# Kernel tuning notes

Measured on AMD Instinct MI355X. Metric: run time of the kernel, lower is better.

The kernel has to match this reference:

```python
import jax, jax.numpy as jnp
import numpy as np

N, F, U, H = 4096, 512, 64, 8
EDGE_PROB = 0.01
NEG_MASK = -10e9  # matches keras-gat masking constant
LRELU_SLOPE = 0.2


def setup_inputs() -> dict:
    key = jax.random.key(0)
    kX, kA, kI, kW, kS, kN, kB = jax.random.split(key, 7)
    X = jax.random.normal(kX, (1, N, F), dtype=jnp.float32)
    # sparse binary adjacency with self loops (layer expects preprocessed self-loops)
    A = (jax.random.uniform(kA, (N, N)) < EDGE_PROB).astype(jnp.float32)
    A = jnp.maximum(A, jnp.eye(N, dtype=jnp.float32))
    out_indices = jax.random.randint(kI, (1, 128), 0, N).astype(jnp.int64)
    scale_w = 1.0 / np.sqrt(F)
    scale_a = 1.0 / np.sqrt(U)
    W = jax.random.normal(kW, (H, F, U), dtype=jnp.float32) * scale_w
    a_self = jax.random.normal(kS, (H, U), dtype=jnp.float32) * scale_a
    a_neigh = jax.random.normal(kN, (H, U), dtype=jnp.float32) * scale_a
    bias = jax.random.normal(kB, (H, U), dtype=jnp.float32) * 0.1
    return {"X": X, "out_indices": out_indices, "A": A, "W": W,
            "a_self": a_self, "a_neigh": a_neigh, "bias": bias}


def reference(X, out_indices, A, W, a_self, a_neigh, bias):
    x = X[0]  # [N, F] (batch dim of 1)
    # per-head linear transform: [H, N, U]
    h = jnp.einsum('nf,hfu->hnu', x, W)
    # additive attention logits: f_self[i] + f_neigh[j]
    f_self = jnp.einsum('hnu,hu->hn', h, a_self)    # [H, N]
    f_neigh = jnp.einsum('hnu,hu->hn', h, a_neigh)  # [H, N]
    scores = f_self[:, :, None] + f_neigh[:, None, :]  # [H, N, N]
    scores = jax.nn.leaky_relu(scores, negative_slope=LRELU_SLOPE)
    # mask non-edges (standard, non-saliency path): dense += -10e9 * (1 - A)
    scores = scores + NEG_MASK * (1.0 - A)[None, :, :]
    attn = jax.nn.softmax(scores, axis=-1)  # [H, N, N]
    # weighted aggregation + bias
    out = jnp.einsum('hnm,hmu->hnu', attn, h) + bias[:, None, :]  # [H, N, U]
    # concat heads: [N, H*U], then activation (relu)
    out = jnp.transpose(out, (1, 0, 2)).reshape(N, H * U)
    out = jax.nn.relu(out)
    return out[None, :, :]  # [1, N, H*U]; final_layer=False -> all nodes
```

## Files before the change

### kernel.cpp

```cpp
#include <hip/hip_runtime.h>
#include <hip/hip_bf16.h>

#define N_NODES 4096
#define F_DIM   512
#define U_DIM   64
#define H_HEADS 8
#define C_DIM   512
#define LRELU_S 0.2f
#define MAXE    128
#define GEMM_BLOCKS 512

typedef __attribute__((ext_vector_type(8))) short bf16x8;
typedef __attribute__((ext_vector_type(4))) float f32x4;

__device__ inline unsigned short f2bf(float f) {
  union { float f; unsigned u; } v; v.f = f;
  unsigned r = v.u + 0x7FFFu + ((v.u >> 16) & 1u);
  return (unsigned short)(r >> 16);
}
__device__ inline float bf2f(unsigned short b) {
  union { unsigned u; float f; } v; v.u = ((unsigned)b) << 16;
  return v.f;
}

__global__ __launch_bounds__(256) void front_kernel(
    const float* __restrict__ X, const float* __restrict__ W,
    const float* __restrict__ A, const float* __restrict__ a_self,
    const float* __restrict__ a_neigh, unsigned short* __restrict__ hb,
    float* __restrict__ fsT, float* __restrict__ fnT, int* __restrict__ deg,
    unsigned short* __restrict__ nbr) {
  __shared__ unsigned short As[64][72];
  __shared__ unsigned short Bs[64][72];
  __shared__ int wsum[4];

  const int t    = threadIdx.x;
  const int lane = t & 63;
  const int w    = t >> 6;

  if ((int)blockIdx.x < GEMM_BLOCKS) {
    const int mblk = blockIdx.x & 63;
    const int head = blockIdx.x >> 6;
    const int m0   = mblk * 64;
    const float* Wh = W + (size_t)head * F_DIM * U_DIM;

    const int wr = w >> 1, wc = w & 1;
    const int arow = t >> 2;
    const int akc  = (t & 3) * 16;
    const int bu   = t & 63;
    const int bjc  = (t >> 6) * 16;

    f32x4 acc[2][2] = {};

    for (int k0 = 0; k0 < F_DIM; k0 += 64) {
      {
        const float* src = X + (size_t)(m0 + arow) * F_DIM + k0 + akc;
        float4 f0 = ((const float4*)src)[0];
        float4 f1 = ((const float4*)src)[1];
        float4 f2 = ((const float4*)src)[2];
        float4 f3 = ((const float4*)src)[3];
        bf16x8 u0 = {(short)f2bf(f0.x), (short)f2bf(f0.y), (short)f2bf(f0.z),
                     (short)f2bf(f0.w), (short)f2bf(f1.x), (short)f2bf(f1.y),
                     (short)f2bf(f1.z), (short)f2bf(f1.w)};
        bf16x8 u1 = {(short)f2bf(f2.x), (short)f2bf(f2.y), (short)f2bf(f2.z),
                     (short)f2bf(f2.w), (short)f2bf(f3.x), (short)f2bf(f3.y),
                     (short)f2bf(f3.z), (short)f2bf(f3.w)};
        *(bf16x8*)&As[arow][akc]     = u0;
        *(bf16x8*)&As[arow][akc + 8] = u1;
      }
      {
        float bv[16];
#pragma unroll
        for (int j = 0; j < 16; ++j)
          bv[j] = Wh[(size_t)(k0 + bjc + j) * U_DIM + bu];
        bf16x8 w0 = {(short)f2bf(bv[0]), (short)f2bf(bv[1]), (short)f2bf(bv[2]),
                     (short)f2bf(bv[3]), (short)f2bf(bv[4]), (short)f2bf(bv[5]),
                     (short)f2bf(bv[6]), (short)f2bf(bv[7])};
        bf16x8 w1 = {(short)f2bf(bv[8]),  (short)f2bf(bv[9]),
                     (short)f2bf(bv[10]), (short)f2bf(bv[11]),
                     (short)f2bf(bv[12]), (short)f2bf(bv[13]),
                     (short)f2bf(bv[14]), (short)f2bf(bv[15])};
        *(bf16x8*)&Bs[bu][bjc]     = w0;
        *(bf16x8*)&Bs[bu][bjc + 8] = w1;
      }
      __syncthreads();

      const int r  = lane & 15;
      const int ko = (lane >> 4) * 8;
#pragma unroll
      for (int kk = 0; kk < 2; ++kk) {
        bf16x8 af0 = *(const bf16x8*)&As[wr * 32 + r][kk * 32 + ko];
        bf16x8 af1 = *(const bf16x8*)&As[wr * 32 + 16 + r][kk * 32 + ko];
        bf16x8 bf0 = *(const bf16x8*)&Bs[wc * 32 + r][kk * 32 + ko];
        bf16x8 bf1 = *(const bf16x8*)&Bs[wc * 32 + 16 + r][kk * 32 + ko];
        acc[0][0] = __builtin_amdgcn_mfma_f32_16x16x32_bf16(af0, bf0, acc[0][0], 0, 0, 0);
        acc[0][1] = __builtin_amdgcn_mfma_f32_16x16x32_bf16(af0, bf1, acc[0][1], 0, 0, 0);
        acc[1][0] = __builtin_amdgcn_mfma_f32_16x16x32_bf16(af1, bf0, acc[1][0], 0, 0, 0);
        acc[1][1] = __builtin_amdgcn_mfma_f32_16x16x32_bf16(af1, bf1, acc[1][1], 0, 0, 0);
      }
      __syncthreads();
    }

#pragma unroll
    for (int mi = 0; mi < 2; ++mi) {
#pragma unroll
      for (int ni = 0; ni < 2; ++ni) {
        const int rb = wr * 32 + mi * 16 + (lane >> 4) * 4;
        const int cl = wc * 32 + ni * 16 + (lane & 15);
#pragma unroll
        for (int reg = 0; reg < 4; ++reg) {
          unsigned short hv = f2bf(acc[mi][ni][reg]);
          hb[(size_t)(m0 + rb + reg) * C_DIM + head * U_DIM + cl] = hv;
          As[rb + reg][cl] = hv;
        }
      }
    }
    __syncthreads();
    if (t < 128) {
      const int r = t & 63;
      const float* avec = (t >= 64) ? a_neigh + head * U_DIM
                                    : a_self + head * U_DIM;
      float s = 0.f;
#pragma unroll
      for (int u = 0; u < 64; ++u) s += bf2f(As[r][u]) * avec[u];
      float* dst = (t >= 64) ? fnT : fsT;
      dst[(size_t)(m0 + r) * H_HEADS + head] = s;
    }
  } else {
    const int i = (int)blockIdx.x - GEMM_BLOCKS;
    const float* Aq = A + (size_t)i * N_NODES + w * 1024;
    float4 v0 = *(const float4*)(Aq +   0 + 4 * lane);
    float4 v1 = *(const float4*)(Aq + 256 + 4 * lane);
    float4 v2 = *(const float4*)(Aq + 512 + 4 * lane);
    float4 v3 = *(const float4*)(Aq + 768 + 4 * lane);

    unsigned long long mk[16];
    mk[ 0] = __ballot(v0.x != 0.f); mk[ 1] = __ballot(v0.y != 0.f);
    mk[ 2] = __ballot(v0.z != 0.f); mk[ 3] = __ballot(v0.w != 0.f);
    mk[ 4] = __ballot(v1.x != 0.f); mk[ 5] = __ballot(v1.y != 0.f);
    mk[ 6] = __ballot(v1.z != 0.f); mk[ 7] = __ballot(v1.w != 0.f);
    mk[ 8] = __ballot(v2.x != 0.f); mk[ 9] = __ballot(v2.y != 0.f);
    mk[10] = __ballot(v2.z != 0.f); mk[11] = __ballot(v2.w != 0.f);
    mk[12] = __ballot(v3.x != 0.f); mk[13] = __ballot(v3.y != 0.f);
    mk[14] = __ballot(v3.z != 0.f); mk[15] = __ballot(v3.w != 0.f);

    int cnt = 0;
#pragma unroll
    for (int q = 0; q < 16; ++q) cnt += __popcll(mk[q]);
    if (lane == 0) wsum[w] = cnt;
    __syncthreads();

    int base = 0;
#pragma unroll
    for (int k = 0; k < 4; ++k)
      if (k < w) base += wsum[k];
    const int total = wsum[0] + wsum[1] + wsum[2] + wsum[3];

    const unsigned long long lt  = (lane == 63) ? 0x7FFFFFFFFFFFFFFFULL
                                                : ((1ULL << lane) - 1ULL);
    const unsigned long long bit = 1ULL << lane;
    unsigned short* nrow = nbr + (size_t)i * MAXE;
#pragma unroll
    for (int q = 0; q < 16; ++q) {
      if (mk[q] & bit) {
        const int pos = base + (int)__popcll(mk[q] & lt);
        if (pos < MAXE)
          nrow[pos] =
              (unsigned short)(w * 1024 + (q >> 2) * 256 + 4 * lane + (q & 3));
      }
      base += (int)__popcll(mk[q]);
    }
    if (t == 0) deg[i] = (total > MAXE) ? MAXE : total;
  }
}

__global__ __launch_bounds__(256) void attn_kernel(
    const unsigned short* __restrict__ hb, const float* __restrict__ fsT,
    const float* __restrict__ fnT, const float* __restrict__ bias,
    const int* __restrict__ deg, const unsigned short* __restrict__ nbr,
    float* __restrict__ out) {
  __shared__ int   eidx[4][MAXE];
  __shared__ float p[4][MAXE][9];

  const int t    = threadIdx.x;
  const int lane = t & 63;
  const int w    = t >> 6;
  const int i    = blockIdx.x * 4 + w;
  const int E    = deg[i];

  float fsv[8];
  {
    float4 a = *(const float4*)(fsT + (size_t)i * H_HEADS);
    float4 b = *(const float4*)(fsT + (size_t)i * H_HEADS + 4);
    fsv[0]=a.x; fsv[1]=a.y; fsv[2]=a.z; fsv[3]=a.w;
    fsv[4]=b.x; fsv[5]=b.y; fsv[6]=b.z; fsv[7]=b.w;
  }

  float pmax[8];
#pragma unroll
  for (int h = 0; h < 8; ++h) pmax[h] = -1e30f;
  for (int e = lane; e < E; e += 64) {
    const int j = (int)nbr[(size_t)i * MAXE + e];
    eidx[w][e] = j;
    float4 a = *(const float4*)(fnT + (size_t)j * H_HEADS);
    float4 b = *(const float4*)(fnT + (size_t)j * H_HEADS + 4);
    float fnv[8] = {a.x, a.y, a.z, a.w, b.x, b.y, b.z, b.w};
#pragma unroll
    for (int h = 0; h < 8; ++h) {
      float sc = fsv[h] + fnv[h];
      sc = (sc > 0.f) ? sc : LRELU_S * sc;
      p[w][e][h] = sc;
      pmax[h] = fmaxf(pmax[h], sc);
    }
  }
#pragma unroll
  for (int h = 0; h < 8; ++h)
#pragma unroll
    for (int off = 32; off > 0; off >>= 1)
      pmax[h] = fmaxf(pmax[h], __shfl_xor(pmax[h], off));

  float psum[8] = {};
  for (int e = lane; e < E; e += 64) {
#pragma unroll
    for (int h = 0; h < 8; ++h) {
      float ex = __expf(p[w][e][h] - pmax[h]);
      p[w][e][h] = ex;
      psum[h] += ex;
    }
  }
#pragma unroll
  for (int h = 0; h < 8; ++h)
#pragma unroll
    for (int off = 32; off > 0; off >>= 1) psum[h] += __shfl_xor(psum[h], off);

  __syncthreads();

  const int cbase = 8 * lane;
  const int hl = lane >> 3;
  float acc[8] = {};
  for (int e = 0; e < E; ++e) {
    const int j = eidx[w][e];
    uint4 v = *(const uint4*)(hb + (size_t)j * C_DIM + cbase);
    const float pe = p[w][e][hl];
    acc[0] += pe * bf2f((unsigned short)(v.x & 0xFFFFu));
    acc[1] += pe * bf2f((unsigned short)(v.x >> 16));
    acc[2] += pe * bf2f((unsigned short)(v.y & 0xFFFFu));
    acc[3] += pe * bf2f((unsigned short)(v.y >> 16));
    acc[4] += pe * bf2f((unsigned short)(v.z & 0xFFFFu));
    acc[5] += pe * bf2f((unsigned short)(v.z >> 16));
    acc[6] += pe * bf2f((unsigned short)(v.w & 0xFFFFu));
    acc[7] += pe * bf2f((unsigned short)(v.w >> 16));
  }
  float sum = psum[0];
#pragma unroll
  for (int h = 1; h < 8; ++h)
    if (hl == h) sum = psum[h];
  const float inv = 1.0f / sum;

  float4 b0 = *(const float4*)(bias + cbase);
  float4 b1 = *(const float4*)(bias + cbase + 4);
  float4 o0, o1;
  o0.x = fmaxf(acc[0] * inv + b0.x, 0.f);
  o0.y = fmaxf(acc[1] * inv + b0.y, 0.f);
  o0.z = fmaxf(acc[2] * inv + b0.z, 0.f);
  o0.w = fmaxf(acc[3] * inv + b0.w, 0.f);
  o1.x = fmaxf(acc[4] * inv + b1.x, 0.f);
  o1.y = fmaxf(acc[5] * inv + b1.y, 0.f);
  o1.z = fmaxf(acc[6] * inv + b1.z, 0.f);
  o1.w = fmaxf(acc[7] * inv + b1.w, 0.f);
  *(float4*)(out + (size_t)i * C_DIM + cbase)     = o0;
  *(float4*)(out + (size_t)i * C_DIM + cbase + 4) = o1;
}

extern "C" void kernel_launch(void* const* d_in, const int* in_sizes, int n_in,
                              void* d_out, int out_size, void* d_ws,
                              size_t ws_size, hipStream_t stream) {
  const float* X       = (const float*)d_in[0];
  const float* A       = (const float*)d_in[2];
  const float* W       = (const float*)d_in[3];
  const float* a_self  = (const float*)d_in[4];
  const float* a_neigh = (const float*)d_in[5];
  const float* bias    = (const float*)d_in[6];
  float* out = (float*)d_out;

  unsigned short* hb = (unsigned short*)d_ws;
  float* fsT = (float*)(hb + (size_t)N_NODES * C_DIM);
  float* fnT = fsT + (size_t)H_HEADS * N_NODES;
  int* deg   = (int*)(fnT + (size_t)H_HEADS * N_NODES);
  unsigned short* nbr = (unsigned short*)(deg + N_NODES);

  front_kernel<<<GEMM_BLOCKS + N_NODES, 256, 0, stream>>>(
      X, W, A, a_self, a_neigh, hb, fsT, fnT, deg, nbr);

  attn_kernel<<<N_NODES / 4, 256, 0, stream>>>(hb, fsT, fnT, bias, deg, nbr,
                                               out);
}
```

Measured before the change: 41.54 us.

## Split each attention node across two wavefronts, each handling four heads

The attention kernel now assigns two wavefronts per destination node instead of one. Each wavefront computes softmax for four of the eight heads and aggregates half of the output columns with 4-wide bf16 loads. This doubles the grid size and halves per-thread serial work, which should expose more memory-level parallelism for the gather. In exchange it adds a block-level sync for neighbor index staging and duplicates some index and score work across the two wavefronts.

Result: slower. 42.99 us (+3.5%).

```diff
diff --git a/kernel.cpp b/kernel.cpp
--- a/kernel.cpp
+++ b/kernel.cpp
@@ -178,97 +178,87 @@
     const float* __restrict__ fnT, const float* __restrict__ bias,
     const int* __restrict__ deg, const unsigned short* __restrict__ nbr,
     float* __restrict__ out) {
-  __shared__ int   eidx[4][MAXE];
-  __shared__ float p[4][MAXE][9];
+  __shared__ int   eidx[2][MAXE];
+  __shared__ float p[2][MAXE][9];
 
   const int t    = threadIdx.x;
   const int lane = t & 63;
   const int w    = t >> 6;
-  const int i    = blockIdx.x * 4 + w;
+  const int nd   = w >> 1;
+  const int wn   = w & 1;
+  const int i    = blockIdx.x * 2 + nd;
   const int E    = deg[i];
 
-  float fsv[8];
   {
-    float4 a = *(const float4*)(fsT + (size_t)i * H_HEADS);
-    float4 b = *(const float4*)(fsT + (size_t)i * H_HEADS + 4);
-    fsv[0]=a.x; fsv[1]=a.y; fsv[2]=a.z; fsv[3]=a.w;
-    fsv[4]=b.x; fsv[5]=b.y; fsv[6]=b.z; fsv[7]=b.w;
-  }
-
-  float pmax[8];
-#pragma unroll
-  for (int h = 0; h < 8; ++h) pmax[h] = -1e30f;
+    const int e = wn * 64 + lane;
+    if (e < E) eidx[nd][e] = (int)nbr[(size_t)i * MAXE + e];
+  }
+  __syncthreads();
+
+  float4 fsq = *(const float4*)(fsT + (size_t)i * H_HEADS + wn * 4);
+  const float fsv[4] = {fsq.x, fsq.y, fsq.z, fsq.w};
+
+  float pmax[4] = {-1e30f, -1e30f, -1e30f, -1e30f};
   for (int e = lane; e < E; e += 64) {
-    const int j = (int)nbr[(size_t)i * MAXE + e];
-    eidx[w][e] = j;
-    float4 a = *(const float4*)(fnT + (size_t)j * H_HEADS);
-    float4 b = *(const float4*)(fnT + (size_t)j * H_HEADS + 4);
-    float fnv[8] = {a.x, a.y, a.z, a.w, b.x, b.y, b.z, b.w};
-#pragma unroll
-    for (int h = 0; h < 8; ++h) {
+    const int j = eidx[nd][e];
+    float4 a = *(const float4*)(fnT + (size_t)j * H_HEADS + wn * 4);
+    float fnv[4] = {a.x, a.y, a.z, a.w};
+#pragma unroll
+    for (int h = 0; h < 4; ++h) {
       float sc = fsv[h] + fnv[h];
       sc = (sc > 0.f) ? sc : LRELU_S * sc;
-      p[w][e][h] = sc;
+      p[nd][e][wn * 4 + h] = sc;
       pmax[h] = fmaxf(pmax[h], sc);
     }
   }
 #pragma unroll
-  for (int h = 0; h < 8; ++h)
+  for (int h = 0; h < 4; ++h)
 #pragma unroll
     for (int off = 32; off > 0; off >>= 1)
       pmax[h] = fmaxf(pmax[h], __shfl_xor(pmax[h], off));
 
-  float psum[8] = {};
+  float psum[4] = {};
   for (int e = lane; e < E; e += 64) {
 #pragma unroll
-    for (int h = 0; h < 8; ++h) {
-      float ex = __expf(p[w][e][h] - pmax[h]);
-      p[w][e][h] = ex;
+    for (int h = 0; h < 4; ++h) {
+      float ex = __expf(p[nd][e][wn * 4 + h] - pmax[h]);
+      p[nd][e][wn * 4 + h] = ex;
       psum[h] += ex;
     }
   }
 #pragma unroll
-  for (int h = 0; h < 8; ++h)
+  for (int h = 0; h < 4; ++h)
 #pragma unroll
     for (int off = 32; off > 0; off >>= 1) psum[h] += __shfl_xor(psum[h], off);
 
   __syncthreads();
 
-  const int cbase = 8 * lane;
-  const int hl = lane >> 3;
-  float acc[8] = {};
+  const int c0 = wn * 256 + 4 * lane;
+  const int hg = lane >> 4;
+  float sum = psum[0];
+#pragma unroll
+  for (int h = 1; h < 4; ++h)
+    if (hg == h) sum = psum[h];
+  const float inv = 1.0f / sum;
+  const int hl = wn * 4 + hg;
+
+  float a0 = 0.f, a1 = 0.f, a2 = 0.f, a3 = 0.f;
   for (int e = 0; e < E; ++e) {
-    const int j = eidx[w][e];
-    uint4 v = *(const uint4*)(hb + (size_t)j * C_DIM + cbase);
-    const float pe = p[w][e][hl];
-    acc[0] += pe * bf2f((unsigned short)(v.x & 0xFFFFu));
-    acc[1] += pe * bf2f((unsigned short)(v.x >> 16));
-    acc[2] += pe * bf2f((unsigned short)(v.y & 0xFFFFu));
-    acc[3] += pe * bf2f((unsigned short)(v.y >> 16));
-    acc[4] += pe * bf2f((unsigned short)(v.z & 0xFFFFu));
-    acc[5] += pe * bf2f((unsigned short)(v.z >> 16));
-    acc[6] += pe * bf2f((unsigned short)(v.w & 0xFFFFu));
-    acc[7] += pe * bf2f((unsigned short)(v.w >> 16));
-  }
-  float sum = psum[0];
-#pragma unroll
-  for (int h = 1; h < 8; ++h)
-    if (hl == h) sum = psum[h];
-  const float inv = 1.0f / sum;
-
-  float4 b0 = *(const float4*)(bias + cbase);
-  float4 b1 = *(const float4*)(bias + cbase + 4);
-  float4 o0, o1;
-  o0.x = fmaxf(acc[0] * inv + b0.x, 0.f);
-  o0.y = fmaxf(acc[1] * inv + b0.y, 0.f);
-  o0.z = fmaxf(acc[2] * inv + b0.z, 0.f);
-  o0.w = fmaxf(acc[3] * inv + b0.w, 0.f);
-  o1.x = fmaxf(acc[4] * inv + b1.x, 0.f);
-  o1.y = fmaxf(acc[5] * inv + b1.y, 0.f);
-  o1.z = fmaxf(acc[6] * inv + b1.z, 0.f);
-  o1.w = fmaxf(acc[7] * inv + b1.w, 0.f);
-  *(float4*)(out + (size_t)i * C_DIM + cbase)     = o0;
-  *(float4*)(out + (size_t)i * C_DIM + cbase + 4) = o1;
+    const int j = eidx[nd][e];
+    uint2 v = *(const uint2*)(hb + (size_t)j * C_DIM + c0);
+    const float pe = p[nd][e][hl];
+    a0 += pe * bf2f((unsigned short)(v.x & 0xFFFFu));
+    a1 += pe * bf2f((unsigned short)(v.x >> 16));
+    a2 += pe * bf2f((unsigned short)(v.y & 0xFFFFu));
+    a3 += pe * bf2f((unsigned short)(v.y >> 16));
+  }
+  float4 bv = *(const float4*)(bias + c0);
+  float4 o;
+  o.x = fmaxf(a0 * inv + bv.x, 0.f);
+  o.y = fmaxf(a1 * inv + bv.y, 0.f);
+  o.z = fmaxf(a2 * inv + bv.z, 0.f);
+  o.w = fmaxf(a3 * inv + bv.w, 0.f);
+  *(float4*)(out + (size_t)i * C_DIM + c0) = o;
 }
 
 extern "C" void kernel_launch(void* const* d_in, const int* in_sizes, int n_in,
@@ -291,6 +281,6 @@
   front_kernel<<<GEMM_BLOCKS + N_NODES, 256, 0, stream>>>(
       X, W, A, a_self, a_neigh, hb, fsT, fnT, deg, nbr);
 
-  attn_kernel<<<N_NODES / 4, 256, 0, stream>>>(hb, fsT, fnT, bias, deg, nbr,
+  attn_kernel<<<N_NODES / 2, 256, 0, stream>>>(hb, fsT, fnT, bias, deg, nbr,
                                                out);
 }
```
